# Kernel optimization log

Measured on AMD Instinct MI355X. Metric: run time of the kernel, lower is better.

Reference implementation:

```python
import jax, jax.numpy as jnp
import numpy as np
import math

NEIGHBOR_RADIUS = 30.0

def _masked_softmax(logits, mask, axis):
    # mask: bool, True = keep; all-masked rows return zeros
    p = jax.nn.softmax(jnp.where(mask, logits, -1e9), axis=axis) * mask.astype(logits.dtype)
    return p / jnp.clip(jnp.sum(p, axis=axis, keepdims=True), 1e-9, None)

def _forward(agents_state, agents_mask, map_polylines, map_poly_mask,
             map_poly_type, map_tl_status, map_on_route,
             pm_w1, pm_b1, pm_w2, pm_b2, type_emb, tl_emb, route_emb,
             mo_w1, mo_b1, mo_w2, mo_b2,
             ae_w1, ae_b1, ae_w2, ae_b2, ae_w3, ae_b3,
             mr_w1, mr_b1, mr_w2, mr_b2,
             nr_w1, nr_b1, nr_w2, nr_b2,
             to_w1, to_b1, to_w2, to_b2):
    relu = jax.nn.relu
    a_mask = (agents_mask > 0.5).astype(agents_state.dtype)   # (B,N,T)
    a_feat = agents_state[..., :5]
    # ---- map polyline node encoder ----
    h = relu(map_polylines @ pm_w1 + pm_b1)                   # (B,M,L,H)
    h = relu(h @ pm_w2 + pm_b2)
    h = h.max(axis=2)                                         # (B,M,H) max-pool over points
    t_idx = jnp.clip(map_poly_type, 0, type_emb.shape[0] - 1)
    s_idx = jnp.clip(map_tl_status, 0, tl_emb.shape[0] - 1)
    r_idx = jnp.clip(map_on_route, 0, route_emb.shape[0] - 1)
    h = h + type_emb[t_idx] + tl_emb[s_idx] + route_emb[r_idx]
    h = relu(h @ mo_w1 + mo_b1) @ mo_w2 + mo_b2
    map_mask = map_poly_mask > 0.5                            # (B,M) bool
    map_node = h * map_mask[..., None].astype(h.dtype)        # (B,M,D)
    map_center = map_polylines.mean(axis=2)                   # (B,M,2)
    # ---- agent state encoder ----
    a = relu(a_feat @ ae_w1 + ae_b1)
    a = relu(a @ ae_w2 + ae_b2)
    a_emb = (a @ ae_w3 + ae_b3) * a_mask[..., None]           # (B,N,T,D)
    D = a_emb.shape[-1]
    # ---- agent -> map attention ----
    agent_pos = a_feat[..., 0:2]
    rel = map_center[:, None, None, :, :] - agent_pos[:, :, :, None, :]  # (B,N,T,M,2)
    dist = jnp.linalg.norm(rel, axis=-1, keepdims=True)
    rel_feat = jnp.concatenate([rel, dist], axis=-1)          # (B,N,T,M,3)
    rel_score = (relu(rel_feat @ mr_w1 + mr_b1) @ mr_w2 + mr_b2)[..., 0]  # (B,N,T,M)
    dot = jnp.einsum('bntd,bmd->bntm', a_emb, map_node) / math.sqrt(D)
    score_mask = jnp.broadcast_to(map_mask[:, None, None, :], dot.shape)
    attn = _masked_softmax(dot + rel_score, score_mask, axis=-1)
    map_ctx = jnp.einsum('bntm,bmd->bntd', attn, map_node)    # (B,N,T,D)
    # ---- neighbor graph attention ----
    pos = a_feat[..., 0:2]
    vel = a_feat[..., 3:5]
    pos_j = jnp.transpose(pos, (0, 2, 1, 3))                  # (B,T,N,2)
    vel_j = jnp.transpose(vel, (0, 2, 1, 3))
    rel_pos = pos_j[:, None, :, :, :] - pos[:, :, :, None, :] # (B,N,T,N,2) = p_j - p_i
    rel_vel = vel_j[:, None, :, :, :] - vel[:, :, :, None, :]
    dist_ij = jnp.linalg.norm(rel_pos, axis=-1, keepdims=True)
    rel_ij = jnp.concatenate([rel_pos, rel_vel, dist_ij], axis=-1)        # (B,N,T,N,5)
    nbr_score = (relu(rel_ij @ nr_w1 + nr_b1) @ nr_w2 + nr_b2)[..., 0]    # (B,N,T,N)
    am_b = agents_mask > 0.5
    valid_i = am_b[..., None]                                 # (B,N,T,1)
    valid_j = jnp.transpose(am_b, (0, 2, 1))[:, None, :, :]   # (B,1,T,N)
    N = pos.shape[1]
    not_self = ~jnp.eye(N, dtype=bool)[None, :, None, :]      # (1,N,1,N)
    nbr_mask = valid_i & valid_j & (dist_ij[..., 0] <= NEIGHBOR_RADIUS) & not_self
    dot_n = jnp.einsum('bitd,bjtd->bitj', a_emb, a_emb) / math.sqrt(D)
    w_n = _masked_softmax(dot_n + nbr_score, nbr_mask, axis=-1)
    nbr_ctx = jnp.einsum('bitj,bjtd->bitd', w_n, a_emb)       # (B,N,T,D)
    # ---- tau head ----
    tau = jnp.concatenate([a_emb, map_ctx, nbr_ctx], axis=-1)
    tau = relu(tau @ to_w1 + to_b1) @ to_w2 + to_b2
    return tau * a_mask[..., None]

def setup_inputs() -> dict:
    key = jax.random.key(0)
    B, N, T, M, L = 2, 32, 32, 256, 20
    H, D, TAU = 128, 128, 64
    ks = jax.random.split(key, 32)
    def f(i, shp):
        return jax.random.normal(ks[i], shp, jnp.float32) * 0.05
    inp = {}
    inp['agents_state'] = jax.random.normal(ks[0], (B, N, T, 5), jnp.float32) * jnp.array([50., 50., 1., 5., 5.], jnp.float32)
    inp['agents_mask'] = jnp.ones((B, N, T), jnp.float32)
    inp['map_polylines'] = jax.random.normal(ks[1], (B, M, L, 2), jnp.float32) * 50.0
    inp['map_poly_mask'] = jnp.ones((B, M), jnp.float32)
    inp['map_poly_type'] = jax.random.randint(ks[2], (B, M), 0, 4)
    inp['map_tl_status'] = jax.random.randint(ks[3], (B, M), 0, 8)
    inp['map_on_route'] = jax.random.randint(ks[4], (B, M), 0, 2)
    inp['pm_w1'] = f(5, (2, H));  inp['pm_b1'] = jnp.zeros((H,), jnp.float32)
    inp['pm_w2'] = f(6, (H, H)); inp['pm_b2'] = jnp.zeros((H,), jnp.float32)
    inp['type_emb'] = f(7, (4, H)); inp['tl_emb'] = f(8, (8, H)); inp['route_emb'] = f(9, (2, H))
    inp['mo_w1'] = f(10, (H, H)); inp['mo_b1'] = jnp.zeros((H,), jnp.float32)
    inp['mo_w2'] = f(11, (H, D)); inp['mo_b2'] = jnp.zeros((D,), jnp.float32)
    inp['ae_w1'] = f(12, (5, H)); inp['ae_b1'] = jnp.zeros((H,), jnp.float32)
    inp['ae_w2'] = f(13, (H, H)); inp['ae_b2'] = jnp.zeros((H,), jnp.float32)
    inp['ae_w3'] = f(14, (H, D)); inp['ae_b3'] = jnp.zeros((D,), jnp.float32)
    inp['mr_w1'] = f(15, (3, H)); inp['mr_b1'] = jnp.zeros((H,), jnp.float32)
    inp['mr_w2'] = f(16, (H, 1)); inp['mr_b2'] = jnp.zeros((1,), jnp.float32)
    inp['nr_w1'] = f(17, (5, H)); inp['nr_b1'] = jnp.zeros((H,), jnp.float32)
    inp['nr_w2'] = f(18, (H, 1)); inp['nr_b2'] = jnp.zeros((1,), jnp.float32)
    inp['to_w1'] = f(19, (3 * D, H)); inp['to_b1'] = jnp.zeros((H,), jnp.float32)
    inp['to_w2'] = f(20, (H, TAU)); inp['to_b2'] = jnp.zeros((TAU,), jnp.float32)
    return inp

def reference(agents_state, agents_mask, map_polylines, map_poly_mask,
              map_poly_type, map_tl_status, map_on_route,
              pm_w1, pm_b1, pm_w2, pm_b2, type_emb, tl_emb, route_emb,
              mo_w1, mo_b1, mo_w2, mo_b2,
              ae_w1, ae_b1, ae_w2, ae_b2, ae_w3, ae_b3,
              mr_w1, mr_b1, mr_w2, mr_b2,
              nr_w1, nr_b1, nr_w2, nr_b2,
              to_w1, to_b1, to_w2, to_b2):
    return _forward(agents_state, agents_mask, map_polylines, map_poly_mask,
                    map_poly_type, map_tl_status, map_on_route,
                    pm_w1, pm_b1, pm_w2, pm_b2, type_emb, tl_emb, route_emb,
                    mo_w1, mo_b1, mo_w2, mo_b2,
                    ae_w1, ae_b1, ae_w2, ae_b2, ae_w3, ae_b3,
                    mr_w1, mr_b1, mr_w2, mr_b2,
                    nr_w1, nr_b1, nr_w2, nr_b2,
                    to_w1, to_b1, to_w2, to_b2)
```

## Files before the change

kernel.cpp:

```cpp
#include <hip/hip_runtime.h>

#define RSQRT_D 0.08838834764831843f

__global__ __launch_bounds__(256) void kAB_front(
    const float* __restrict__ poly, const float* __restrict__ pmask,
    const int* __restrict__ ptype, const int* __restrict__ ptl, const int* __restrict__ proute,
    const float* __restrict__ pm_w1, const float* __restrict__ pm_b1,
    const float* __restrict__ pm_w2, const float* __restrict__ pm_b2,
    const float* __restrict__ type_emb, const float* __restrict__ tl_emb, const float* __restrict__ route_emb,
    const float* __restrict__ mo_w1, const float* __restrict__ mo_b1,
    const float* __restrict__ mo_w2, const float* __restrict__ mo_b2,
    const float* __restrict__ astate, const float* __restrict__ amask,
    const float* __restrict__ ae_w1, const float* __restrict__ ae_b1,
    const float* __restrict__ ae_w2, const float* __restrict__ ae_b2,
    const float* __restrict__ ae_w3, const float* __restrict__ ae_b3,
    float* __restrict__ map_node, float* __restrict__ map_nodeT, float* __restrict__ center,
    float* __restrict__ a_emb, float* __restrict__ aT, float* __restrict__ posT)
{
    int tid = threadIdx.x;
    if (blockIdx.x < 512) {
        int bm = blockIdx.x;
        int b = bm >> 8, m = bm & 255;
        int h = tid & 127, rw = tid >> 7;
        __shared__ float xch[2][128];
        __shared__ __align__(16) float hvs[128];
        __shared__ __align__(16) float g2[128];
        __shared__ __align__(16) float h1s[2][128][12];

        {
            int k = h;
            int half = rw;
            const float* pp = poly + bm*40 + half*20;
            float wx = pm_w1[k], wy = pm_w1[128+k], bb = pm_b1[k];
            float h1v[10];
            #pragma unroll
            for (int u = 0; u < 10; ++u) {
                float x = pp[2*u], y = pp[2*u+1];
                h1v[u] = fmaxf(fmaf(wx, x, fmaf(wy, y, bb)), 0.f);
            }
            float4 s0 = make_float4(h1v[0], h1v[1], h1v[2], h1v[3]);
            float4 s1 = make_float4(h1v[4], h1v[5], h1v[6], h1v[7]);
            float2 s2 = make_float2(h1v[8], h1v[9]);
            *(float4*)&h1s[half][k][0] = s0;
            *(float4*)&h1s[half][k][4] = s1;
            *(float2*)&h1s[half][k][8] = s2;
        }
        __syncthreads();

        float acc[10];
        #pragma unroll
        for (int u = 0; u < 10; ++u) acc[u] = 0.f;
        const float* w2p = pm_w2 + h;
        #pragma unroll 2
        for (int k = 0; k < 128; ++k) {
            float w2v = w2p[k*128];
            float4 A  = *(const float4*)&h1s[rw][k][0];
            float4 Bv = *(const float4*)&h1s[rw][k][4];
            float2 Cv = *(const float2*)&h1s[rw][k][8];
            acc[0] = fmaf(A.x,  w2v, acc[0]);
            acc[1] = fmaf(A.y,  w2v, acc[1]);
            acc[2] = fmaf(A.z,  w2v, acc[2]);
            acc[3] = fmaf(A.w,  w2v, acc[3]);
            acc[4] = fmaf(Bv.x, w2v, acc[4]);
            acc[5] = fmaf(Bv.y, w2v, acc[5]);
            acc[6] = fmaf(Bv.z, w2v, acc[6]);
            acc[7] = fmaf(Bv.w, w2v, acc[7]);
            acc[8] = fmaf(Cv.x, w2v, acc[8]);
            acc[9] = fmaf(Cv.y, w2v, acc[9]);
        }
        float mx = acc[0];
        #pragma unroll
        for (int u = 1; u < 10; ++u) mx = fmaxf(mx, acc[u]);
        xch[rw][h] = mx;
        __syncthreads();
        if (rw == 0) {
            float v = fmaxf(fmaxf(mx, xch[1][h]) + pm_b2[h], 0.f);
            int ti = min(max(ptype[bm],0),3);
            int si = min(max(ptl[bm],0),7);
            int ri = min(max(proute[bm],0),1);
            hvs[h] = v + type_emb[ti*128+h] + tl_emb[si*128+h] + route_emb[ri*128+h];
        }
        __syncthreads();
        if (rw == 0) {
            float a1 = mo_b1[h];
            for (int kc = 0; kc < 32; ++kc) {
                float4 xv = *(const float4*)&hvs[kc*4];
                a1 = fmaf(xv.x, mo_w1[(kc*4+0)*128+h],
                     fmaf(xv.y, mo_w1[(kc*4+1)*128+h],
                     fmaf(xv.z, mo_w1[(kc*4+2)*128+h],
                     fmaf(xv.w, mo_w1[(kc*4+3)*128+h], a1))));
            }
            g2[h] = fmaxf(a1, 0.f);
        }
        __syncthreads();
        if (rw == 0) {
            float a2 = mo_b2[h];
            for (int kc = 0; kc < 32; ++kc) {
                float4 xv = *(const float4*)&g2[kc*4];
                a2 = fmaf(xv.x, mo_w2[(kc*4+0)*128+h],
                     fmaf(xv.y, mo_w2[(kc*4+1)*128+h],
                     fmaf(xv.z, mo_w2[(kc*4+2)*128+h],
                     fmaf(xv.w, mo_w2[(kc*4+3)*128+h], a2))));
            }
            float mk = (pmask[bm] > 0.5f) ? 1.f : 0.f;
            a2 *= mk;
            map_node[bm*128 + h] = a2;
            map_nodeT[(b*128+h)*256 + m] = a2;
        }
        if (tid == 0) {
            float sx = 0.f, sy = 0.f;
            #pragma unroll
            for (int l = 0; l < 20; ++l) { sx += poly[bm*40 + 2*l]; sy += poly[bm*40 + 2*l + 1]; }
            center[bm*2+0] = sx * 0.05f;
            center[bm*2+1] = sy * 0.05f;
        }
    } else {
        int h = tid & 127, rp = tid >> 7;
        int r0 = (blockIdx.x - 512)*8 + rp*4;
        __shared__ float f5[2][4][5];
        __shared__ __align__(16) float a1s[2][4][128];
        if (h < 20) f5[rp][h/5][h%5] = astate[(r0 + h/5)*5 + (h%5)];
        __syncthreads();
        float b1v = ae_b1[h];
        float v[4];
        {
            float w0 = ae_w1[h], w1 = ae_w1[128+h], w2 = ae_w1[256+h], w3 = ae_w1[384+h], w4 = ae_w1[512+h];
            #pragma unroll
            for (int r = 0; r < 4; ++r) {
                float a = b1v;
                a = fmaf(f5[rp][r][0], w0, a); a = fmaf(f5[rp][r][1], w1, a);
                a = fmaf(f5[rp][r][2], w2, a); a = fmaf(f5[rp][r][3], w3, a);
                a = fmaf(f5[rp][r][4], w4, a);
                v[r] = fmaxf(a, 0.f);
            }
        }
        #pragma unroll
        for (int r = 0; r < 4; ++r) a1s[rp][r][h] = v[r];
        __syncthreads();
        {
            float b2v = ae_b2[h];
            float a0 = b2v, a1 = b2v, a2 = b2v, a3 = b2v;
            for (int kc = 0; kc < 32; ++kc) {
                float4 x0 = *(const float4*)&a1s[rp][0][kc*4];
                float4 x1 = *(const float4*)&a1s[rp][1][kc*4];
                float4 x2 = *(const float4*)&a1s[rp][2][kc*4];
                float4 x3 = *(const float4*)&a1s[rp][3][kc*4];
                float w0 = ae_w2[(kc*4+0)*128+h], w1 = ae_w2[(kc*4+1)*128+h];
                float w2 = ae_w2[(kc*4+2)*128+h], w3 = ae_w2[(kc*4+3)*128+h];
                a0 = fmaf(x0.x,w0,fmaf(x0.y,w1,fmaf(x0.z,w2,fmaf(x0.w,w3,a0))));
                a1 = fmaf(x1.x,w0,fmaf(x1.y,w1,fmaf(x1.z,w2,fmaf(x1.w,w3,a1))));
                a2 = fmaf(x2.x,w0,fmaf(x2.y,w1,fmaf(x2.z,w2,fmaf(x2.w,w3,a2))));
                a3 = fmaf(x3.x,w0,fmaf(x3.y,w1,fmaf(x3.z,w2,fmaf(x3.w,w3,a3))));
            }
            v[0]=fmaxf(a0,0.f); v[1]=fmaxf(a1,0.f); v[2]=fmaxf(a2,0.f); v[3]=fmaxf(a3,0.f);
        }
        __syncthreads();
        #pragma unroll
        for (int r = 0; r < 4; ++r) a1s[rp][r][h] = v[r];
        __syncthreads();
        {
            float b3v = ae_b3[h];
            float a0 = b3v, a1 = b3v, a2 = b3v, a3 = b3v;
            for (int kc = 0; kc < 32; ++kc) {
                float4 x0 = *(const float4*)&a1s[rp][0][kc*4];
                float4 x1 = *(const float4*)&a1s[rp][1][kc*4];
                float4 x2 = *(const float4*)&a1s[rp][2][kc*4];
                float4 x3 = *(const float4*)&a1s[rp][3][kc*4];
                float w0 = ae_w3[(kc*4+0)*128+h], w1 = ae_w3[(kc*4+1)*128+h];
                float w2 = ae_w3[(kc*4+2)*128+h], w3 = ae_w3[(kc*4+3)*128+h];
                a0 = fmaf(x0.x,w0,fmaf(x0.y,w1,fmaf(x0.z,w2,fmaf(x0.w,w3,a0))));
                a1 = fmaf(x1.x,w0,fmaf(x1.y,w1,fmaf(x1.z,w2,fmaf(x1.w,w3,a1))));
                a2 = fmaf(x2.x,w0,fmaf(x2.y,w1,fmaf(x2.z,w2,fmaf(x2.w,w3,a2))));
                a3 = fmaf(x3.x,w0,fmaf(x3.y,w1,fmaf(x3.z,w2,fmaf(x3.w,w3,a3))));
            }
            v[0]=a0; v[1]=a1; v[2]=a2; v[3]=a3;
        }
        #pragma unroll
        for (int r = 0; r < 4; ++r) {
            int rr = r0 + r;
            float mk = (amask[rr] > 0.5f) ? 1.f : 0.f;
            float e = v[r] * mk;
            a_emb[rr*128 + h] = e;
            int bb = rr >> 10, nn = (rr >> 5) & 31, tt = rr & 31;
            int bt = bb*32 + tt;
            aT[(bt*128 + h)*32 + nn] = e;
        }
        if (h < 20) {
            int r = h / 5, c = h % 5;
            int rr = r0 + r;
            int bb = rr >> 10, nn = (rr >> 5) & 31, tt = rr & 31;
            int bt = bb*32 + tt;
            float val;
            if      (c == 0) val = f5[rp][r][0];
            else if (c == 1) val = f5[rp][r][1];
            else if (c == 2) val = f5[rp][r][3];
            else if (c == 3) val = f5[rp][r][4];
            else             val = amask[rr];
            posT[(bt*5 + c)*32 + nn] = val;
        }
    }
}

__global__ __launch_bounds__(512) void kCD_fused(
    const float* __restrict__ astate, const float* __restrict__ amask,
    const float* __restrict__ pmask,
    const float* __restrict__ a_emb, const float* __restrict__ map_node,
    const float* __restrict__ map_nodeT, const float* __restrict__ center,
    const float* __restrict__ mr_w1, const float* __restrict__ mr_b1,
    const float* __restrict__ mr_w2, const float* __restrict__ mr_b2,
    const float* __restrict__ aT, const float* __restrict__ posT,
    const float* __restrict__ nr_w1, const float* __restrict__ nr_b1,
    const float* __restrict__ nr_w2, const float* __restrict__ nr_b2,
    const float* __restrict__ to_w1, const float* __restrict__ to_b1,
    const float* __restrict__ to_w2, const float* __restrict__ to_b2,
    float* __restrict__ out)
{
    int tid = threadIdx.x;
    int r0 = blockIdx.x * 4;
    int b = r0 >> 10, t0 = r0 & 31;

    __shared__ float lg4[4][256];
    __shared__ __align__(16) float p4[256*4];
    __shared__ float ctxp[4][128];
    __shared__ float pj[4][32];
    __shared__ __align__(16) float tau[4][384];
    __shared__ float redn[4][128];
    __shared__ __align__(16) float gpart[4][4][128];
    __shared__ __align__(16) float g1s[4][128];

    if (tid < 256) {
        int m = tid;
        float rx[4], ry[4], dd[4], dt[4], sA[4];
        float b2c = mr_b2[0];
        float cx = center[(b*256+m)*2+0], cy = center[(b*256+m)*2+1];
        #pragma unroll
        for (int r = 0; r < 4; ++r) {
            float px = astate[(r0+r)*5+0], py = astate[(r0+r)*5+1];
            rx[r] = cx - px; ry[r] = cy - py;
            dd[r] = sqrtf(rx[r]*rx[r] + ry[r]*ry[r]);
            dt[r] = 0.f; sA[r] = b2c;
        }
        #pragma unroll 8
        for (int hh = 0; hh < 128; ++hh) {
            float wa = mr_w1[hh], wb = mr_w1[128+hh], wc = mr_w1[256+hh];
            float bb = mr_b1[hh], w2 = mr_w2[hh];
            #pragma unroll
            for (int r = 0; r < 4; ++r) {
                float t1 = fmaf(rx[r], wa, fmaf(ry[r], wb, fmaf(dd[r], wc, bb)));
                sA[r] = fmaf(fmaxf(t1, 0.f), w2, sA[r]);
            }
        }
        const float* mT = map_nodeT + b*128*256 + m;
        #pragma unroll 8
        for (int d = 0; d < 128; ++d) {
            float v = mT[d*256];
            #pragma unroll
            for (int r = 0; r < 4; ++r)
                dt[r] = fmaf(v, a_emb[(r0+r)*128 + d], dt[r]);
        }
        bool mk = pmask[b*256+m] > 0.5f;
        #pragma unroll
        for (int r = 0; r < 4; ++r)
            lg4[r][m] = mk ? fmaf(dt[r], RSQRT_D, sA[r]) : -1e30f;
    } else {
        int lam = tid & 63, wv = (tid >> 6) & 3;
        int r = r0 + wv;
        int ii = (r >> 5) & 31, tt = r & 31;
        int bt = b*32 + tt;
        int j = lam & 31, hs = lam >> 5;
        float pxi = astate[r*5+0], pyi = astate[r*5+1], vxi = astate[r*5+3], vyi = astate[r*5+4];
        const float* pT = posT + bt*160;
        float pxj = pT[j], pyj = pT[32+j], vxj = pT[64+j], vyj = pT[96+j], mj = pT[128+j];
        float rpx = pxj-pxi, rpy = pyj-pyi, rvx = vxj-vxi, rvy = vyj-vyi;
        float ddv = sqrtf(rpx*rpx + rpy*rpy);
        const float* ei = a_emb + (size_t)r*128;
        const float* aTp = aT + (size_t)bt*4096 + j;
        float s = 0.f, dot = 0.f;
        int h0 = hs*64;
        #pragma unroll 8
        for (int q = 0; q < 64; ++q) {
            int hh = h0 + q;
            float wA = nr_w1[hh], wB = nr_w1[128+hh], wC = nr_w1[256+hh];
            float wD = nr_w1[384+hh], wE = nr_w1[512+hh];
            float bb = nr_b1[hh], w2 = nr_w2[hh];
            float t1 = fmaf(rpx, wA, fmaf(rpy, wB, fmaf(rvx, wC,
                       fmaf(rvy, wD, fmaf(ddv, wE, bb)))));
            s = fmaf(fmaxf(t1, 0.f), w2, s);
            dot = fmaf(ei[hh], aTp[hh*32], dot);
        }
        s   += __shfl_xor(s, 32);
        dot += __shfl_xor(dot, 32);
        bool vi = amask[r] > 0.5f, vj = mj > 0.5f;
        bool ok = vi && vj && (ddv <= 30.0f) && (j != ii);
        float lg = ok ? fmaf(dot, RSQRT_D, s + nr_b2[0]) : -1e30f;
        float mxv = lg;
        #pragma unroll
        for (int off = 16; off; off >>= 1) mxv = fmaxf(mxv, __shfl_xor(mxv, off));
        float e = (lg > -1e29f) ? expf(lg - mxv) : 0.f;
        float sm = e;
        #pragma unroll
        for (int off = 16; off; off >>= 1) sm += __shfl_xor(sm, off);
        if (hs == 0) pj[wv][j] = e / fmaxf(sm, 1e-9f);
    }
    __syncthreads();

    if (tid < 256) {
        int lam = tid & 63, wv = tid >> 6;
        float x0 = lg4[wv][lam], x1 = lg4[wv][64+lam], x2 = lg4[wv][128+lam], x3 = lg4[wv][192+lam];
        float mxv = fmaxf(fmaxf(x0,x1), fmaxf(x2,x3));
        #pragma unroll
        for (int off = 32; off; off >>= 1) mxv = fmaxf(mxv, __shfl_xor(mxv, off));
        float e0 = (x0 > -1e29f) ? expf(x0-mxv) : 0.f;
        float e1 = (x1 > -1e29f) ? expf(x1-mxv) : 0.f;
        float e2 = (x2 > -1e29f) ? expf(x2-mxv) : 0.f;
        float e3 = (x3 > -1e29f) ? expf(x3-mxv) : 0.f;
        float sm = e0+e1+e2+e3;
        #pragma unroll
        for (int off = 32; off; off >>= 1) sm += __shfl_xor(sm, off);
        float inv = 1.f / fmaxf(sm, 1e-9f);
        p4[lam*4 + wv]       = e0*inv;
        p4[(64+lam)*4 + wv]  = e1*inv;
        p4[(128+lam)*4 + wv] = e2*inv;
        p4[(192+lam)*4 + wv] = e3*inv;
    } else {
        int idx = tid - 256;
        int d = idx & 127, rr = idx >> 7;
        tau[rr][d]   = a_emb[(r0+rr)*128 + d];
        tau[rr+2][d] = a_emb[(r0+rr+2)*128 + d];
    }
    __syncthreads();

    float pv0 = 0.f, pv1 = 0.f, pv2 = 0.f, pv3 = 0.f;
    if (tid < 256) {
        int d = tid & 127, hf = tid >> 7;
        const float* mn = map_node + (b*256 + hf*128)*128 + d;
        const float4* ppv = (const float4*)p4 + hf*128;
        #pragma unroll 4
        for (int mm = 0; mm < 128; ++mm) {
            float4 pvv = ppv[mm];
            float v = mn[mm*128];
            pv0 = fmaf(pvv.x, v, pv0); pv1 = fmaf(pvv.y, v, pv1);
            pv2 = fmaf(pvv.z, v, pv2); pv3 = fmaf(pvv.w, v, pv3);
        }
        if (hf == 1) { ctxp[0][d]=pv0; ctxp[1][d]=pv1; ctxp[2][d]=pv2; ctxp[3][d]=pv3; }
    }
    __syncthreads();
    if (tid < 128) {
        int d = tid;
        tau[0][128+d] = pv0 + ctxp[0][d];
        tau[1][128+d] = pv1 + ctxp[1][d];
        tau[2][128+d] = pv2 + ctxp[2][d];
        tau[3][128+d] = pv3 + ctxp[3][d];
    }
    __syncthreads();

    float na0 = 0.f, na1 = 0.f, na2 = 0.f, na3 = 0.f;
    if (tid < 256) {
        int d = tid & 127, hf = tid >> 7;
        for (int jj = 0; jj < 16; ++jj) {
            int j2 = hf*16 + jj;
            float p0 = pj[0][j2], p1 = pj[1][j2], p2 = pj[2][j2], p3 = pj[3][j2];
            const float* ejb = a_emb + (size_t)((b*32 + j2)*32 + t0)*128 + d;
            na0 = fmaf(p0, ejb[0],   na0);
            na1 = fmaf(p1, ejb[128], na1);
            na2 = fmaf(p2, ejb[256], na2);
            na3 = fmaf(p3, ejb[384], na3);
        }
        if (hf == 1) { redn[0][d]=na0; redn[1][d]=na1; redn[2][d]=na2; redn[3][d]=na3; }
    }
    __syncthreads();
    if (tid < 128) {
        int d = tid;
        tau[0][256+d] = na0 + redn[0][d];
        tau[1][256+d] = na1 + redn[1][d];
        tau[2][256+d] = na2 + redn[2][d];
        tau[3][256+d] = na3 + redn[3][d];
    }
    __syncthreads();

    if (tid < 256) {
        int h6 = tid & 63, kq = tid >> 6;
        float aL[4] = {0.f,0.f,0.f,0.f};
        float aH[4] = {0.f,0.f,0.f,0.f};
        for (int c = 0; c < 24; ++c) {
            int k4 = kq*24 + c;
            float4 x0 = *(const float4*)&tau[0][k4*4];
            float4 x1 = *(const float4*)&tau[1][k4*4];
            float4 x2 = *(const float4*)&tau[2][k4*4];
            float4 x3 = *(const float4*)&tau[3][k4*4];
            float wl0 = to_w1[(k4*4+0)*128 + h6], wh0 = to_w1[(k4*4+0)*128 + 64+h6];
            float wl1 = to_w1[(k4*4+1)*128 + h6], wh1 = to_w1[(k4*4+1)*128 + 64+h6];
            float wl2 = to_w1[(k4*4+2)*128 + h6], wh2 = to_w1[(k4*4+2)*128 + 64+h6];
            float wl3 = to_w1[(k4*4+3)*128 + h6], wh3 = to_w1[(k4*4+3)*128 + 64+h6];
            aL[0]=fmaf(x0.x,wl0,fmaf(x0.y,wl1,fmaf(x0.z,wl2,fmaf(x0.w,wl3,aL[0]))));
            aH[0]=fmaf(x0.x,wh0,fmaf(x0.y,wh1,fmaf(x0.z,wh2,fmaf(x0.w,wh3,aH[0]))));
            aL[1]=fmaf(x1.x,wl0,fmaf(x1.y,wl1,fmaf(x1.z,wl2,fmaf(x1.w,wl3,aL[1]))));
            aH[1]=fmaf(x1.x,wh0,fmaf(x1.y,wh1,fmaf(x1.z,wh2,fmaf(x1.w,wh3,aH[1]))));
            aL[2]=fmaf(x2.x,wl0,fmaf(x2.y,wl1,fmaf(x2.z,wl2,fmaf(x2.w,wl3,aL[2]))));
            aH[2]=fmaf(x2.x,wh0,fmaf(x2.y,wh1,fmaf(x2.z,wh2,fmaf(x2.w,wh3,aH[2]))));
            aL[3]=fmaf(x3.x,wl0,fmaf(x3.y,wl1,fmaf(x3.z,wl2,fmaf(x3.w,wl3,aL[3]))));
            aH[3]=fmaf(x3.x,wh0,fmaf(x3.y,wh1,fmaf(x3.z,wh2,fmaf(x3.w,wh3,aH[3]))));
        }
        #pragma unroll
        for (int r = 0; r < 4; ++r) {
            gpart[kq][r][h6]      = aL[r];
            gpart[kq][r][64 + h6] = aH[r];
        }
    }
    __syncthreads();
    if (tid < 256) {
        int h = tid & 127, rp = tid >> 7;
        float bv = to_b1[h];
        #pragma unroll
        for (int rr = rp; rr < 4; rr += 2) {
            float s = gpart[0][rr][h] + gpart[1][rr][h] + gpart[2][rr][h] + gpart[3][rr][h];
            g1s[rr][h] = fmaxf(s + bv, 0.f);
        }
    }
    __syncthreads();
    if (tid < 256) {
        int o = tid & 63, row = tid >> 6;
        float a2 = to_b2[o];
        for (int kc = 0; kc < 32; ++kc) {
            float4 g = *(const float4*)&g1s[row][kc*4];
            a2 = fmaf(g.x, to_w2[(kc*4+0)*64 + o],
                 fmaf(g.y, to_w2[(kc*4+1)*64 + o],
                 fmaf(g.z, to_w2[(kc*4+2)*64 + o],
                 fmaf(g.w, to_w2[(kc*4+3)*64 + o], a2))));
        }
        float mk = (amask[r0+row] > 0.5f) ? 1.f : 0.f;
        out[(r0+row)*64 + o] = a2 * mk;
    }
}

extern "C" void kernel_launch(void* const* d_in, const int* in_sizes, int n_in,
                              void* d_out, int out_size, void* d_ws, size_t ws_size,
                              hipStream_t stream) {
    const float* agents_state  = (const float*)d_in[0];
    const float* agents_mask   = (const float*)d_in[1];
    const float* map_polylines = (const float*)d_in[2];
    const float* map_poly_mask = (const float*)d_in[3];
    const int*   map_poly_type = (const int*)d_in[4];
    const int*   map_tl_status = (const int*)d_in[5];
    const int*   map_on_route  = (const int*)d_in[6];
    const float* pm_w1 = (const float*)d_in[7];
    const float* pm_b1 = (const float*)d_in[8];
    const float* pm_w2 = (const float*)d_in[9];
    const float* pm_b2 = (const float*)d_in[10];
    const float* type_emb  = (const float*)d_in[11];
    const float* tl_emb    = (const float*)d_in[12];
    const float* route_emb = (const float*)d_in[13];
    const float* mo_w1 = (const float*)d_in[14];
    const float* mo_b1 = (const float*)d_in[15];
    const float* mo_w2 = (const float*)d_in[16];
    const float* mo_b2 = (const float*)d_in[17];
    const float* ae_w1 = (const float*)d_in[18];
    const float* ae_b1 = (const float*)d_in[19];
    const float* ae_w2 = (const float*)d_in[20];
    const float* ae_b2 = (const float*)d_in[21];
    const float* ae_w3 = (const float*)d_in[22];
    const float* ae_b3 = (const float*)d_in[23];
    const float* mr_w1 = (const float*)d_in[24];
    const float* mr_b1 = (const float*)d_in[25];
    const float* mr_w2 = (const float*)d_in[26];
    const float* mr_b2 = (const float*)d_in[27];
    const float* nr_w1 = (const float*)d_in[28];
    const float* nr_b1 = (const float*)d_in[29];
    const float* nr_w2 = (const float*)d_in[30];
    const float* nr_b2 = (const float*)d_in[31];
    const float* to_w1 = (const float*)d_in[32];
    const float* to_b1 = (const float*)d_in[33];
    const float* to_w2 = (const float*)d_in[34];
    const float* to_b2 = (const float*)d_in[35];

    float* ws = (float*)d_ws;
    float* map_node  = ws;
    float* map_nodeT = ws + 65536;
    float* center    = ws + 131072;
    float* a_emb     = ws + 132096;
    float* aT        = ws + 394240;
    float* posT      = ws + 656384;

    float* out = (float*)d_out;

    kAB_front<<<768, 256, 0, stream>>>(map_polylines, map_poly_mask,
        map_poly_type, map_tl_status, map_on_route,
        pm_w1, pm_b1, pm_w2, pm_b2, type_emb, tl_emb, route_emb,
        mo_w1, mo_b1, mo_w2, mo_b2,
        agents_state, agents_mask,
        ae_w1, ae_b1, ae_w2, ae_b2, ae_w3, ae_b3,
        map_node, map_nodeT, center, a_emb, aT, posT);

    kCD_fused<<<512, 512, 0, stream>>>(agents_state, agents_mask, map_poly_mask,
        a_emb, map_node, map_nodeT, center,
        mr_w1, mr_b1, mr_w2, mr_b2,
        aT, posT,
        nr_w1, nr_b1, nr_w2, nr_b2,
        to_w1, to_b1, to_w2, to_b2,
        out);
}
```

Measured before the change: 195.9 us.

## Halve rows per block in fused attention kernel and rebalance thread roles

Each block of the fused agent kernel now handles 2 agent rows instead of 4, and the grid doubles to 1024 blocks. All 512 threads compute map logits, one row per 256 threads, with the relation MLP and dot product merged into one loop. The map-context and neighbor-context reductions run at the same time on separate thread halves, which removes two barriers, and the output MLP's K dimension is split 8 ways. This buys more parallelism and shorter serial chains, at the cost of less reuse of weights and map_node loads across rows, since each row now reloads mr_w1 and map_node.

```diff
diff --git a/kernel.cpp b/kernel.cpp
--- a/kernel.cpp
+++ b/kernel.cpp
@@ -216,54 +216,42 @@
     float* __restrict__ out)
 {
     int tid = threadIdx.x;
-    int r0 = blockIdx.x * 4;
+    int r0 = blockIdx.x * 2;
     int b = r0 >> 10, t0 = r0 & 31;
 
-    __shared__ float lg4[4][256];
-    __shared__ __align__(16) float p4[256*4];
-    __shared__ float ctxp[4][128];
-    __shared__ float pj[4][32];
-    __shared__ __align__(16) float tau[4][384];
-    __shared__ float redn[4][128];
-    __shared__ __align__(16) float gpart[4][4][128];
-    __shared__ __align__(16) float g1s[4][128];
-
-    if (tid < 256) {
-        int m = tid;
-        float rx[4], ry[4], dd[4], dt[4], sA[4];
+    __shared__ float lg4[2][256];
+    __shared__ __align__(16) float p4[256*2];
+    __shared__ float ctxp[2][128];
+    __shared__ float pj[2][32];
+    __shared__ __align__(16) float tau[2][384];
+    __shared__ float redn[2][128];
+    __shared__ __align__(16) float gpart[8][2][128];
+    __shared__ __align__(16) float g1s[2][128];
+
+    {
+        int m = tid & 255, row = tid >> 8;
+        int r = r0 + row;
         float b2c = mr_b2[0];
         float cx = center[(b*256+m)*2+0], cy = center[(b*256+m)*2+1];
-        #pragma unroll
-        for (int r = 0; r < 4; ++r) {
-            float px = astate[(r0+r)*5+0], py = astate[(r0+r)*5+1];
-            rx[r] = cx - px; ry[r] = cy - py;
-            dd[r] = sqrtf(rx[r]*rx[r] + ry[r]*ry[r]);
-            dt[r] = 0.f; sA[r] = b2c;
-        }
+        float px = astate[r*5+0], py = astate[r*5+1];
+        float rx = cx - px, ry = cy - py;
+        float dd = sqrtf(rx*rx + ry*ry);
+        float dt = 0.f, sA = b2c;
+        const float* mT = map_nodeT + b*128*256 + m;
+        const float* ae = a_emb + (size_t)r*128;
         #pragma unroll 8
         for (int hh = 0; hh < 128; ++hh) {
             float wa = mr_w1[hh], wb = mr_w1[128+hh], wc = mr_w1[256+hh];
             float bb = mr_b1[hh], w2 = mr_w2[hh];
-            #pragma unroll
-            for (int r = 0; r < 4; ++r) {
-                float t1 = fmaf(rx[r], wa, fmaf(ry[r], wb, fmaf(dd[r], wc, bb)));
-                sA[r] = fmaf(fmaxf(t1, 0.f), w2, sA[r]);
-            }
-        }
-        const float* mT = map_nodeT + b*128*256 + m;
-        #pragma unroll 8
-        for (int d = 0; d < 128; ++d) {
-            float v = mT[d*256];
-            #pragma unroll
-            for (int r = 0; r < 4; ++r)
-                dt[r] = fmaf(v, a_emb[(r0+r)*128 + d], dt[r]);
+            float t1 = fmaf(rx, wa, fmaf(ry, wb, fmaf(dd, wc, bb)));
+            sA = fmaf(fmaxf(t1, 0.f), w2, sA);
+            dt = fmaf(mT[hh*256], ae[hh], dt);
         }
         bool mk = pmask[b*256+m] > 0.5f;
-        #pragma unroll
-        for (int r = 0; r < 4; ++r)
-            lg4[r][m] = mk ? fmaf(dt[r], RSQRT_D, sA[r]) : -1e30f;
-    } else {
-        int lam = tid & 63, wv = (tid >> 6) & 3;
+        lg4[row][m] = mk ? fmaf(dt, RSQRT_D, sA) : -1e30f;
+    }
+    if (tid < 128) {
+        int lam = tid & 63, wv = tid >> 6;
         int r = r0 + wv;
         int ii = (r >> 5) & 31, tt = r & 31;
         int bt = b*32 + tt;
@@ -301,10 +289,14 @@
         #pragma unroll
         for (int off = 16; off; off >>= 1) sm += __shfl_xor(sm, off);
         if (hs == 0) pj[wv][j] = e / fmaxf(sm, 1e-9f);
-    }
-    __syncthreads();
-
-    if (tid < 256) {
+    } else if (tid < 256) {
+        int d = tid - 128;
+        tau[0][d] = a_emb[(size_t)r0*128 + d];
+        tau[1][d] = a_emb[(size_t)(r0+1)*128 + d];
+    }
+    __syncthreads();
+
+    if (tid < 128) {
         int lam = tid & 63, wv = tid >> 6;
         float x0 = lg4[wv][lam], x1 = lg4[wv][64+lam], x2 = lg4[wv][128+lam], x3 = lg4[wv][192+lam];
         float mxv = fmaxf(fmaxf(x0,x1), fmaxf(x2,x3));
@@ -318,107 +310,83 @@
         #pragma unroll
         for (int off = 32; off; off >>= 1) sm += __shfl_xor(sm, off);
         float inv = 1.f / fmaxf(sm, 1e-9f);
-        p4[lam*4 + wv]       = e0*inv;
-        p4[(64+lam)*4 + wv]  = e1*inv;
-        p4[(128+lam)*4 + wv] = e2*inv;
-        p4[(192+lam)*4 + wv] = e3*inv;
-    } else {
-        int idx = tid - 256;
-        int d = idx & 127, rr = idx >> 7;
-        tau[rr][d]   = a_emb[(r0+rr)*128 + d];
-        tau[rr+2][d] = a_emb[(r0+rr+2)*128 + d];
-    }
-    __syncthreads();
-
-    float pv0 = 0.f, pv1 = 0.f, pv2 = 0.f, pv3 = 0.f;
+        p4[lam*2 + wv]       = e0*inv;
+        p4[(64+lam)*2 + wv]  = e1*inv;
+        p4[(128+lam)*2 + wv] = e2*inv;
+        p4[(192+lam)*2 + wv] = e3*inv;
+    }
+    __syncthreads();
+
+    float pv0 = 0.f, pv1 = 0.f;
+    float na0 = 0.f, na1 = 0.f;
     if (tid < 256) {
         int d = tid & 127, hf = tid >> 7;
         const float* mn = map_node + (b*256 + hf*128)*128 + d;
-        const float4* ppv = (const float4*)p4 + hf*128;
-        #pragma unroll 4
+        const float2* ppv = (const float2*)p4 + hf*128;
+        #pragma unroll 8
         for (int mm = 0; mm < 128; ++mm) {
-            float4 pvv = ppv[mm];
+            float2 pvv = ppv[mm];
             float v = mn[mm*128];
             pv0 = fmaf(pvv.x, v, pv0); pv1 = fmaf(pvv.y, v, pv1);
-            pv2 = fmaf(pvv.z, v, pv2); pv3 = fmaf(pvv.w, v, pv3);
-        }
-        if (hf == 1) { ctxp[0][d]=pv0; ctxp[1][d]=pv1; ctxp[2][d]=pv2; ctxp[3][d]=pv3; }
-    }
-    __syncthreads();
+        }
+        if (hf == 1) { ctxp[0][d]=pv0; ctxp[1][d]=pv1; }
+    } else {
+        int local = tid - 256;
+        int d = local & 127, hf = local >> 7;
+        for (int jj = 0; jj < 16; ++jj) {
+            int j2 = hf*16 + jj;
+            float p0 = pj[0][j2], p1 = pj[1][j2];
+            const float* ejb = a_emb + (size_t)((b*32 + j2)*32 + t0)*128 + d;
+            na0 = fmaf(p0, ejb[0],   na0);
+            na1 = fmaf(p1, ejb[128], na1);
+        }
+        if (hf == 1) { redn[0][d]=na0; redn[1][d]=na1; }
+    }
+    __syncthreads();
+
     if (tid < 128) {
         int d = tid;
         tau[0][128+d] = pv0 + ctxp[0][d];
         tau[1][128+d] = pv1 + ctxp[1][d];
-        tau[2][128+d] = pv2 + ctxp[2][d];
-        tau[3][128+d] = pv3 + ctxp[3][d];
-    }
-    __syncthreads();
-
-    float na0 = 0.f, na1 = 0.f, na2 = 0.f, na3 = 0.f;
-    if (tid < 256) {
-        int d = tid & 127, hf = tid >> 7;
-        for (int jj = 0; jj < 16; ++jj) {
-            int j2 = hf*16 + jj;
-            float p0 = pj[0][j2], p1 = pj[1][j2], p2 = pj[2][j2], p3 = pj[3][j2];
-            const float* ejb = a_emb + (size_t)((b*32 + j2)*32 + t0)*128 + d;
-            na0 = fmaf(p0, ejb[0],   na0);
-            na1 = fmaf(p1, ejb[128], na1);
-            na2 = fmaf(p2, ejb[256], na2);
-            na3 = fmaf(p3, ejb[384], na3);
-        }
-        if (hf == 1) { redn[0][d]=na0; redn[1][d]=na1; redn[2][d]=na2; redn[3][d]=na3; }
-    }
-    __syncthreads();
-    if (tid < 128) {
-        int d = tid;
+    } else if (tid >= 256 && tid < 384) {
+        int d = tid - 256;
         tau[0][256+d] = na0 + redn[0][d];
         tau[1][256+d] = na1 + redn[1][d];
-        tau[2][256+d] = na2 + redn[2][d];
-        tau[3][256+d] = na3 + redn[3][d];
-    }
-    __syncthreads();
-
-    if (tid < 256) {
+    }
+    __syncthreads();
+
+    {
         int h6 = tid & 63, kq = tid >> 6;
-        float aL[4] = {0.f,0.f,0.f,0.f};
-        float aH[4] = {0.f,0.f,0.f,0.f};
-        for (int c = 0; c < 24; ++c) {
-            int k4 = kq*24 + c;
+        float aL0=0.f, aH0=0.f, aL1=0.f, aH1=0.f;
+        for (int c = 0; c < 12; ++c) {
+            int k4 = kq*12 + c;
             float4 x0 = *(const float4*)&tau[0][k4*4];
             float4 x1 = *(const float4*)&tau[1][k4*4];
-            float4 x2 = *(const float4*)&tau[2][k4*4];
-            float4 x3 = *(const float4*)&tau[3][k4*4];
             float wl0 = to_w1[(k4*4+0)*128 + h6], wh0 = to_w1[(k4*4+0)*128 + 64+h6];
             float wl1 = to_w1[(k4*4+1)*128 + h6], wh1 = to_w1[(k4*4+1)*128 + 64+h6];
             float wl2 = to_w1[(k4*4+2)*128 + h6], wh2 = to_w1[(k4*4+2)*128 + 64+h6];
             float wl3 = to_w1[(k4*4+3)*128 + h6], wh3 = to_w1[(k4*4+3)*128 + 64+h6];
-            aL[0]=fmaf(x0.x,wl0,fmaf(x0.y,wl1,fmaf(x0.z,wl2,fmaf(x0.w,wl3,aL[0]))));
-            aH[0]=fmaf(x0.x,wh0,fmaf(x0.y,wh1,fmaf(x0.z,wh2,fmaf(x0.w,wh3,aH[0]))));
-            aL[1]=fmaf(x1.x,wl0,fmaf(x1.y,wl1,fmaf(x1.z,wl2,fmaf(x1.w,wl3,aL[1]))));
-            aH[1]=fmaf(x1.x,wh0,fmaf(x1.y,wh1,fmaf(x1.z,wh2,fmaf(x1.w,wh3,aH[1]))));
-            aL[2]=fmaf(x2.x,wl0,fmaf(x2.y,wl1,fmaf(x2.z,wl2,fmaf(x2.w,wl3,aL[2]))));
-            aH[2]=fmaf(x2.x,wh0,fmaf(x2.y,wh1,fmaf(x2.z,wh2,fmaf(x2.w,wh3,aH[2]))));
-            aL[3]=fmaf(x3.x,wl0,fmaf(x3.y,wl1,fmaf(x3.z,wl2,fmaf(x3.w,wl3,aL[3]))));
-            aH[3]=fmaf(x3.x,wh0,fmaf(x3.y,wh1,fmaf(x3.z,wh2,fmaf(x3.w,wh3,aH[3]))));
-        }
-        #pragma unroll
-        for (int r = 0; r < 4; ++r) {
-            gpart[kq][r][h6]      = aL[r];
-            gpart[kq][r][64 + h6] = aH[r];
-        }
-    }
-    __syncthreads();
+            aL0=fmaf(x0.x,wl0,fmaf(x0.y,wl1,fmaf(x0.z,wl2,fmaf(x0.w,wl3,aL0))));
+            aH0=fmaf(x0.x,wh0,fmaf(x0.y,wh1,fmaf(x0.z,wh2,fmaf(x0.w,wh3,aH0))));
+            aL1=fmaf(x1.x,wl0,fmaf(x1.y,wl1,fmaf(x1.z,wl2,fmaf(x1.w,wl3,aL1))));
+            aH1=fmaf(x1.x,wh0,fmaf(x1.y,wh1,fmaf(x1.z,wh2,fmaf(x1.w,wh3,aH1))));
+        }
+        gpart[kq][0][h6]      = aL0;
+        gpart[kq][0][64 + h6] = aH0;
+        gpart[kq][1][h6]      = aL1;
+        gpart[kq][1][64 + h6] = aH1;
+    }
+    __syncthreads();
+
     if (tid < 256) {
-        int h = tid & 127, rp = tid >> 7;
-        float bv = to_b1[h];
-        #pragma unroll
-        for (int rr = rp; rr < 4; rr += 2) {
-            float s = gpart[0][rr][h] + gpart[1][rr][h] + gpart[2][rr][h] + gpart[3][rr][h];
-            g1s[rr][h] = fmaxf(s + bv, 0.f);
-        }
-    }
-    __syncthreads();
-    if (tid < 256) {
+        int h = tid & 127, rr = tid >> 7;
+        float s = gpart[0][rr][h] + gpart[1][rr][h] + gpart[2][rr][h] + gpart[3][rr][h]
+                + gpart[4][rr][h] + gpart[5][rr][h] + gpart[6][rr][h] + gpart[7][rr][h];
+        g1s[rr][h] = fmaxf(s + to_b1[h], 0.f);
+    }
+    __syncthreads();
+
+    if (tid < 128) {
         int o = tid & 63, row = tid >> 6;
         float a2 = to_b2[o];
         for (int kc = 0; kc < 32; ++kc) {
@@ -491,7 +459,7 @@
         ae_w1, ae_b1, ae_w2, ae_b2, ae_w3, ae_b3,
         map_node, map_nodeT, center, a_emb, aT, posT);
 
-    kCD_fused<<<512, 512, 0, stream>>>(agents_state, agents_mask, map_poly_mask,
+    kCD_fused<<<1024, 512, 0, stream>>>(agents_state, agents_mask, map_poly_mask,
         a_emb, map_node, map_nodeT, center,
         mr_w1, mr_b1, mr_w2, mr_b2,
         aT, posT,
```

Measured after the change: 199.2 us. About the same (+1.7%).

## Spread idle-thread work across full block in map MLP and attention tail

Applied to the files above, without the earlier changes.

In the map-node encoder, the two 128x128 MLP layers are split across both 128-thread halves by K, with partial sums reduced through shared memory instead of leaving half the block idle. In the attention kernel, the rel-score MLP loop and the map dot-product loop are fused into one pass. The map-context and neighbor-aggregation reductions now run concurrently on different thread groups, removing a barrier phase. The to_w1 GEMV is spread over all 512 threads. This adds extra shared-memory reductions and barriers in the map encoder.

```diff
diff --git a/kernel.cpp b/kernel.cpp
--- a/kernel.cpp
+++ b/kernel.cpp
@@ -81,31 +81,40 @@
             hvs[h] = v + type_emb[ti*128+h] + tl_emb[si*128+h] + route_emb[ri*128+h];
         }
         __syncthreads();
-        if (rw == 0) {
-            float a1 = mo_b1[h];
-            for (int kc = 0; kc < 32; ++kc) {
-                float4 xv = *(const float4*)&hvs[kc*4];
-                a1 = fmaf(xv.x, mo_w1[(kc*4+0)*128+h],
-                     fmaf(xv.y, mo_w1[(kc*4+1)*128+h],
-                     fmaf(xv.z, mo_w1[(kc*4+2)*128+h],
-                     fmaf(xv.w, mo_w1[(kc*4+3)*128+h], a1))));
+        {
+            float a1 = (rw == 0) ? mo_b1[h] : 0.f;
+            int k0 = rw * 64;
+            for (int kc = 0; kc < 16; ++kc) {
+                float4 xv = *(const float4*)&hvs[k0 + kc*4];
+                a1 = fmaf(xv.x, mo_w1[(k0+kc*4+0)*128+h],
+                     fmaf(xv.y, mo_w1[(k0+kc*4+1)*128+h],
+                     fmaf(xv.z, mo_w1[(k0+kc*4+2)*128+h],
+                     fmaf(xv.w, mo_w1[(k0+kc*4+3)*128+h], a1))));
             }
-            g2[h] = fmaxf(a1, 0.f);
-        }
-        __syncthreads();
-        if (rw == 0) {
-            float a2 = mo_b2[h];
-            for (int kc = 0; kc < 32; ++kc) {
-                float4 xv = *(const float4*)&g2[kc*4];
-                a2 = fmaf(xv.x, mo_w2[(kc*4+0)*128+h],
-                     fmaf(xv.y, mo_w2[(kc*4+1)*128+h],
-                     fmaf(xv.z, mo_w2[(kc*4+2)*128+h],
-                     fmaf(xv.w, mo_w2[(kc*4+3)*128+h], a2))));
+            xch[rw][h] = a1;
+        }
+        __syncthreads();
+        if (tid < 128) g2[tid] = fmaxf(xch[0][tid] + xch[1][tid], 0.f);
+        __syncthreads();
+        {
+            float a2 = (rw == 0) ? mo_b2[h] : 0.f;
+            int k0 = rw * 64;
+            for (int kc = 0; kc < 16; ++kc) {
+                float4 xv = *(const float4*)&g2[k0 + kc*4];
+                a2 = fmaf(xv.x, mo_w2[(k0+kc*4+0)*128+h],
+                     fmaf(xv.y, mo_w2[(k0+kc*4+1)*128+h],
+                     fmaf(xv.z, mo_w2[(k0+kc*4+2)*128+h],
+                     fmaf(xv.w, mo_w2[(k0+kc*4+3)*128+h], a2))));
             }
+            xch[rw][h] = a2;
+        }
+        __syncthreads();
+        if (tid < 128) {
+            float a2 = xch[0][tid] + xch[1][tid];
             float mk = (pmask[bm] > 0.5f) ? 1.f : 0.f;
             a2 *= mk;
-            map_node[bm*128 + h] = a2;
-            map_nodeT[(b*128+h)*256 + m] = a2;
+            map_node[bm*128 + tid] = a2;
+            map_nodeT[(b*128+tid)*256 + m] = a2;
         }
         if (tid == 0) {
             float sx = 0.f, sy = 0.f;
@@ -240,23 +249,28 @@
             dd[r] = sqrtf(rx[r]*rx[r] + ry[r]*ry[r]);
             dt[r] = 0.f; sA[r] = b2c;
         }
-        #pragma unroll 8
+        const float* mT = map_nodeT + b*128*256 + m;
+        const float* ae0 = a_emb + (size_t)(r0+0)*128;
+        const float* ae1 = a_emb + (size_t)(r0+1)*128;
+        const float* ae2 = a_emb + (size_t)(r0+2)*128;
+        const float* ae3 = a_emb + (size_t)(r0+3)*128;
+        #pragma unroll 4
         for (int hh = 0; hh < 128; ++hh) {
             float wa = mr_w1[hh], wb = mr_w1[128+hh], wc = mr_w1[256+hh];
             float bb = mr_b1[hh], w2 = mr_w2[hh];
-            #pragma unroll
-            for (int r = 0; r < 4; ++r) {
-                float t1 = fmaf(rx[r], wa, fmaf(ry[r], wb, fmaf(dd[r], wc, bb)));
-                sA[r] = fmaf(fmaxf(t1, 0.f), w2, sA[r]);
-            }
-        }
-        const float* mT = map_nodeT + b*128*256 + m;
-        #pragma unroll 8
-        for (int d = 0; d < 128; ++d) {
-            float v = mT[d*256];
-            #pragma unroll
-            for (int r = 0; r < 4; ++r)
-                dt[r] = fmaf(v, a_emb[(r0+r)*128 + d], dt[r]);
+            float v = mT[hh*256];
+            float t10 = fmaf(rx[0], wa, fmaf(ry[0], wb, fmaf(dd[0], wc, bb)));
+            float t11 = fmaf(rx[1], wa, fmaf(ry[1], wb, fmaf(dd[1], wc, bb)));
+            float t12 = fmaf(rx[2], wa, fmaf(ry[2], wb, fmaf(dd[2], wc, bb)));
+            float t13 = fmaf(rx[3], wa, fmaf(ry[3], wb, fmaf(dd[3], wc, bb)));
+            sA[0] = fmaf(fmaxf(t10, 0.f), w2, sA[0]);
+            sA[1] = fmaf(fmaxf(t11, 0.f), w2, sA[1]);
+            sA[2] = fmaf(fmaxf(t12, 0.f), w2, sA[2]);
+            sA[3] = fmaf(fmaxf(t13, 0.f), w2, sA[3]);
+            dt[0] = fmaf(v, ae0[hh], dt[0]);
+            dt[1] = fmaf(v, ae1[hh], dt[1]);
+            dt[2] = fmaf(v, ae2[hh], dt[2]);
+            dt[3] = fmaf(v, ae3[hh], dt[3]);
         }
         bool mk = pmask[b*256+m] > 0.5f;
         #pragma unroll
@@ -325,12 +339,13 @@
     } else {
         int idx = tid - 256;
         int d = idx & 127, rr = idx >> 7;
-        tau[rr][d]   = a_emb[(r0+rr)*128 + d];
-        tau[rr+2][d] = a_emb[(r0+rr+2)*128 + d];
+        tau[rr][d]   = a_emb[(size_t)(r0+rr)*128 + d];
+        tau[rr+2][d] = a_emb[(size_t)(r0+rr+2)*128 + d];
     }
     __syncthreads();
 
     float pv0 = 0.f, pv1 = 0.f, pv2 = 0.f, pv3 = 0.f;
+    float na0 = 0.f, na1 = 0.f, na2 = 0.f, na3 = 0.f;
     if (tid < 256) {
         int d = tid & 127, hf = tid >> 7;
         const float* mn = map_node + (b*256 + hf*128)*128 + d;
@@ -343,20 +358,9 @@
             pv2 = fmaf(pvv.z, v, pv2); pv3 = fmaf(pvv.w, v, pv3);
         }
         if (hf == 1) { ctxp[0][d]=pv0; ctxp[1][d]=pv1; ctxp[2][d]=pv2; ctxp[3][d]=pv3; }
-    }
-    __syncthreads();
-    if (tid < 128) {
-        int d = tid;
-        tau[0][128+d] = pv0 + ctxp[0][d];
-        tau[1][128+d] = pv1 + ctxp[1][d];
-        tau[2][128+d] = pv2 + ctxp[2][d];
-        tau[3][128+d] = pv3 + ctxp[3][d];
-    }
-    __syncthreads();
-
-    float na0 = 0.f, na1 = 0.f, na2 = 0.f, na3 = 0.f;
-    if (tid < 256) {
-        int d = tid & 127, hf = tid >> 7;
+    } else {
+        int local = tid - 256;
+        int d = local & 127, hf = local >> 7;
         for (int jj = 0; jj < 16; ++jj) {
             int j2 = hf*16 + jj;
             float p0 = pj[0][j2], p1 = pj[1][j2], p2 = pj[2][j2], p3 = pj[3][j2];
@@ -369,8 +373,15 @@
         if (hf == 1) { redn[0][d]=na0; redn[1][d]=na1; redn[2][d]=na2; redn[3][d]=na3; }
     }
     __syncthreads();
+
     if (tid < 128) {
         int d = tid;
+        tau[0][128+d] = pv0 + ctxp[0][d];
+        tau[1][128+d] = pv1 + ctxp[1][d];
+        tau[2][128+d] = pv2 + ctxp[2][d];
+        tau[3][128+d] = pv3 + ctxp[3][d];
+    } else if (tid >= 256 && tid < 384) {
+        int d = tid - 256;
         tau[0][256+d] = na0 + redn[0][d];
         tau[1][256+d] = na1 + redn[1][d];
         tau[2][256+d] = na2 + redn[2][d];
@@ -378,46 +389,39 @@
     }
     __syncthreads();
 
-    if (tid < 256) {
-        int h6 = tid & 63, kq = tid >> 6;
-        float aL[4] = {0.f,0.f,0.f,0.f};
-        float aH[4] = {0.f,0.f,0.f,0.f};
+    {
+        int h6 = tid & 63, kq = (tid >> 6) & 3, side = tid >> 8;
+        int col = side*64 + h6;
+        float a0v = 0.f, a1v = 0.f, a2v = 0.f, a3v = 0.f;
         for (int c = 0; c < 24; ++c) {
             int k4 = kq*24 + c;
             float4 x0 = *(const float4*)&tau[0][k4*4];
             float4 x1 = *(const float4*)&tau[1][k4*4];
             float4 x2 = *(const float4*)&tau[2][k4*4];
             float4 x3 = *(const float4*)&tau[3][k4*4];
-            float wl0 = to_w1[(k4*4+0)*128 + h6], wh0 = to_w1[(k4*4+0)*128 + 64+h6];
-            float wl1 = to_w1[(k4*4+1)*128 + h6], wh1 = to_w1[(k4*4+1)*128 + 64+h6];
-            float wl2 = to_w1[(k4*4+2)*128 + h6], wh2 = to_w1[(k4*4+2)*128 + 64+h6];
-            float wl3 = to_w1[(k4*4+3)*128 + h6], wh3 = to_w1[(k4*4+3)*128 + 64+h6];
-            aL[0]=fmaf(x0.x,wl0,fmaf(x0.y,wl1,fmaf(x0.z,wl2,fmaf(x0.w,wl3,aL[0]))));
-            aH[0]=fmaf(x0.x,wh0,fmaf(x0.y,wh1,fmaf(x0.z,wh2,fmaf(x0.w,wh3,aH[0]))));
-            aL[1]=fmaf(x1.x,wl0,fmaf(x1.y,wl1,fmaf(x1.z,wl2,fmaf(x1.w,wl3,aL[1]))));
-            aH[1]=fmaf(x1.x,wh0,fmaf(x1.y,wh1,fmaf(x1.z,wh2,fmaf(x1.w,wh3,aH[1]))));
-            aL[2]=fmaf(x2.x,wl0,fmaf(x2.y,wl1,fmaf(x2.z,wl2,fmaf(x2.w,wl3,aL[2]))));
-            aH[2]=fmaf(x2.x,wh0,fmaf(x2.y,wh1,fmaf(x2.z,wh2,fmaf(x2.w,wh3,aH[2]))));
-            aL[3]=fmaf(x3.x,wl0,fmaf(x3.y,wl1,fmaf(x3.z,wl2,fmaf(x3.w,wl3,aL[3]))));
-            aH[3]=fmaf(x3.x,wh0,fmaf(x3.y,wh1,fmaf(x3.z,wh2,fmaf(x3.w,wh3,aH[3]))));
-        }
-        #pragma unroll
-        for (int r = 0; r < 4; ++r) {
-            gpart[kq][r][h6]      = aL[r];
-            gpart[kq][r][64 + h6] = aH[r];
-        }
+            float w0 = to_w1[(k4*4+0)*128 + col];
+            float w1 = to_w1[(k4*4+1)*128 + col];
+            float w2 = to_w1[(k4*4+2)*128 + col];
+            float w3 = to_w1[(k4*4+3)*128 + col];
+            a0v = fmaf(x0.x,w0,fmaf(x0.y,w1,fmaf(x0.z,w2,fmaf(x0.w,w3,a0v))));
+            a1v = fmaf(x1.x,w0,fmaf(x1.y,w1,fmaf(x1.z,w2,fmaf(x1.w,w3,a1v))));
+            a2v = fmaf(x2.x,w0,fmaf(x2.y,w1,fmaf(x2.z,w2,fmaf(x2.w,w3,a2v))));
+            a3v = fmaf(x3.x,w0,fmaf(x3.y,w1,fmaf(x3.z,w2,fmaf(x3.w,w3,a3v))));
+        }
+        gpart[kq][0][col] = a0v;
+        gpart[kq][1][col] = a1v;
+        gpart[kq][2][col] = a2v;
+        gpart[kq][3][col] = a3v;
     }
     __syncthreads();
-    if (tid < 256) {
-        int h = tid & 127, rp = tid >> 7;
-        float bv = to_b1[h];
-        #pragma unroll
-        for (int rr = rp; rr < 4; rr += 2) {
-            float s = gpart[0][rr][h] + gpart[1][rr][h] + gpart[2][rr][h] + gpart[3][rr][h];
-            g1s[rr][h] = fmaxf(s + bv, 0.f);
-        }
+
+    {
+        int h = tid & 127, rr = tid >> 7;
+        float s = gpart[0][rr][h] + gpart[1][rr][h] + gpart[2][rr][h] + gpart[3][rr][h];
+        g1s[rr][h] = fmaxf(s + to_b1[h], 0.f);
     }
     __syncthreads();
+
     if (tid < 256) {
         int o = tid & 63, row = tid >> 6;
         float a2 = to_b2[o];
```

Result: faster. 179.5 us (median of 2 runs) (-8.4%).
